# Kernel optimization log

Hardware: AMD Instinct MI355X
Metric: run time of the kernel (lower is better)

## Reference

```python
import jax, jax.numpy as jnp
import numpy as np

N = 50000      # nodes
E = 800000     # edges (before self-loops)
IN = 128       # in_channels
HID = 32       # hidden_channels per head
H = 4          # in_head
OUT = 40       # out_channels
OH = 1         # out_head
NEG = 0.2      # GATConv default negative_slope
EPS = 1e-5     # BatchNorm eps
SKIP = 0.5     # skip_coefficient


def setup_inputs() -> dict:
    key = jax.random.key(0)
    ks = jax.random.split(key, 24)
    s = 0.1
    f32 = jnp.float32
    return dict(
        x=jax.random.normal(ks[0], (N, IN), dtype=f32),
        W0=jax.random.normal(ks[1], (H * HID, IN), dtype=f32) * s,
        as0=jax.random.normal(ks[2], (H, HID), dtype=f32) * s,
        ad0=jax.random.normal(ks[3], (H, HID), dtype=f32) * s,
        b0=jnp.zeros((H * HID,), f32),
        g0=jnp.ones((H * HID,), f32),
        be0=jnp.zeros((H * HID,), f32),
        W1=jax.random.normal(ks[4], (H * HID, H * HID), dtype=f32) * s,
        as1=jax.random.normal(ks[5], (H, HID), dtype=f32) * s,
        ad1=jax.random.normal(ks[6], (H, HID), dtype=f32) * s,
        b1=jnp.zeros((H * HID,), f32),
        g1=jnp.ones((H * HID,), f32),
        be1=jnp.zeros((H * HID,), f32),
        W2=jax.random.normal(ks[7], (OH * OUT, H * HID), dtype=f32) * s,
        as2=jax.random.normal(ks[8], (OH, OUT), dtype=f32) * s,
        ad2=jax.random.normal(ks[9], (OH, OUT), dtype=f32) * s,
        b2=jnp.zeros((OH * OUT,), f32),
        edge_index=jax.random.randint(ks[10], (2, E), 0, N, dtype=jnp.int64),
    )


def gat_layer(x, src, dst, W, a_s, a_d, b, heads, ch):
    # PyG GATConv (concat=True): per-head linear, edge LeakyReLU attention,
    # softmax over incoming edges per destination node, scatter-add aggregate.
    n = x.shape[0]
    h = (x @ W.T).reshape(n, heads, ch)            # [N,H,C]
    al_s = jnp.einsum('nhc,hc->nh', h, a_s)        # [N,H]
    al_d = jnp.einsum('nhc,hc->nh', h, a_d)
    e = jax.nn.leaky_relu(al_s[src] + al_d[dst], NEG)   # [Etot,H]
    m = jax.ops.segment_max(e, dst, num_segments=n)     # per-dst max (stable softmax)
    ex = jnp.exp(e - m[dst])
    denom = jax.ops.segment_sum(ex, dst, num_segments=n)
    alpha = ex / denom[dst]                              # [Etot,H]
    out = jax.ops.segment_sum(alpha[:, :, None] * h[src], dst, num_segments=n)
    return out.reshape(n, heads * ch) + b


def batchnorm(x, g, b):
    # BatchNorm1d, batch-statistics form
    mu = x.mean(0)
    var = x.var(0)
    return (x - mu) * jax.lax.rsqrt(var + EPS) * g + b


def reference(x, W0, as0, ad0, b0, g0, be0, W1, as1, ad1, b1, g1, be1,
              W2, as2, ad2, b2, edge_index):
    loops = jnp.arange(N, dtype=edge_index.dtype)   # GATConv add_self_loops=True
    src = jnp.concatenate([edge_index[0], loops])
    dst = jnp.concatenate([edge_index[1], loops])
    h = jax.nn.relu(batchnorm(gat_layer(x, src, dst, W0, as0, ad0, b0, H, HID), g0, be0))
    skip = h
    h = gat_layer(h, src, dst, W1, as1, ad1, b1, H, HID)
    h = jax.nn.relu(batchnorm(h, g1, be1) + SKIP * skip)
    return gat_layer(h, src, dst, W2, as2, ad2, b2, OH, OUT)
```

## Files before the change

kernel.cpp:

```cpp
#include <hip/hip_runtime.h>
#include <hip/hip_bf16.h>
#include <stdint.h>

#define N_NODES 50000
#define N_EDGES 800000
#define TOT_EDGES (N_EDGES + N_NODES)
#define DIM 128
#define NEG 0.2f
#define BN_EPS 1e-5f
#define SKIPC 0.5f
#define NB 196
#define BCAP 6144
#define BINA_BLKS ((N_EDGES + 4095) / 4096)

typedef __attribute__((ext_vector_type(8))) short short8;
typedef __attribute__((ext_vector_type(4))) float f32x4;

__device__ inline float bf2f(__hip_bfloat16 v) { return __bfloat162float(v); }
__device__ inline float u16f(unsigned short u) { return __uint_as_float(((unsigned int)u) << 16); }
__device__ inline unsigned short f2bu(float f) {
    __hip_bfloat16 b = __float2bfloat16(f);
    return *(unsigned short*)&b;
}
__device__ inline void fma8(float* acc, float ex, uint4 u) {
    acc[0] += ex * u16f((unsigned short)(u.x & 0xFFFFu));
    acc[1] += ex * u16f((unsigned short)(u.x >> 16));
    acc[2] += ex * u16f((unsigned short)(u.y & 0xFFFFu));
    acc[3] += ex * u16f((unsigned short)(u.y >> 16));
    acc[4] += ex * u16f((unsigned short)(u.z & 0xFFFFu));
    acc[5] += ex * u16f((unsigned short)(u.z >> 16));
    acc[6] += ex * u16f((unsigned short)(u.w & 0xFFFFu));
    acc[7] += ex * u16f((unsigned short)(u.w >> 16));
}
__device__ inline unsigned int pk2(float a, float b) {
    return (unsigned int)f2bu(a) | ((unsigned int)f2bu(b) << 16);
}

__global__ void zero_out_k(unsigned short* out, int n) {
    int g = blockIdx.x * 256 + threadIdx.x;
    if (g < n) out[g] = 0;
}

__device__ inline void binA_body(int bid, const int* __restrict__ ei,
                                 int* __restrict__ bcnt,
                                 unsigned int* __restrict__ pairs) {
    __shared__ int cnt[NB], base[NB], cur[NB];
    __shared__ int sf;
    int t = threadIdx.x;
    if (t == 0) sf = 0;
    for (int i = t; i < NB; i += 256) cnt[i] = 0;
    __syncthreads();
    if (t < 16 && ei[2 * t + 1] != 0) atomicOr(&sf, 1);
    __syncthreads();
    int f = (sf == 0);
    int b0 = bid * 4096;
    unsigned int pk[16];
    int bk[16];
    #pragma unroll
    for (int j = 0; j < 16; ++j) {
        int g = b0 + j * 256 + t;
        bk[j] = -1;
        if (g < N_EDGES) {
            int s, d;
            if (f) { s = ei[2 * g]; d = ei[2 * (N_EDGES + g)]; }
            else   { s = ei[g];     d = ei[N_EDGES + g]; }
            if ((unsigned)d < N_NODES && (unsigned)s < N_NODES) {
                bk[j] = d >> 8;
                pk[j] = (unsigned int)s | ((unsigned int)(d & 255) << 16);
                atomicAdd(&cnt[bk[j]], 1);
            }
        }
    }
    __syncthreads();
    if (t < NB) {
        int c = cnt[t];
        base[t] = c ? atomicAdd(&bcnt[t], c) : 0;
        cur[t] = 0;
    }
    __syncthreads();
    #pragma unroll
    for (int j = 0; j < 16; ++j) {
        if (bk[j] >= 0) {
            int off = base[bk[j]] + atomicAdd(&cur[bk[j]], 1);
            if (off < BCAP) pairs[(size_t)bk[j] * BCAP + off] = pk[j];
        }
    }
}

struct PrepJobs { const void* src[13]; float* dst[13]; int n[13]; };
__device__ inline void wcvt_body(int bid,
                                 const void* __restrict__ W0,
                                 const void* __restrict__ W1,
                                 const void* __restrict__ W2,
                                 unsigned short* __restrict__ Wb0,
                                 unsigned short* __restrict__ Wb1,
                                 unsigned short* __restrict__ Wb2,
                                 const PrepJobs& jobs,
                                 int* __restrict__ fflag) {
    __shared__ int cs;
    int t = threadIdx.x;
    if (t == 0) cs = 0;
    __syncthreads();
    {
        unsigned int w = ((const unsigned int*)W0)[t];
        float v0 = u16f((unsigned short)(w & 0xFFFFu));
        float a = fabsf(v0);
        int sane = (a < 2.0f && (a > 1e-20f || v0 == 0.0f)) ? 1 : 0;
        atomicAdd(&cs, sane);
    }
    __syncthreads();
    int f = (cs >= 128) ? 1 : 0;
    if (bid == 0 && t == 0) fflag[0] = f;
    if (bid < 148) {
        int g = bid * 256 + t;
        const void* W; unsigned short* Wb; int idx;
        if (g < 16384)        { W = W0; Wb = Wb0; idx = g; }
        else if (g < 32768)   { W = W1; Wb = Wb1; idx = g - 16384; }
        else if (g < 37888)   { W = W2; Wb = Wb2; idx = g - 32768; }
        else return;
        if (f) Wb[idx] = ((const unsigned short*)W)[idx];
        else   Wb[idx] = f2bu(((const float*)W)[idx]);
    } else {
        int j = bid - 148;
        int n = jobs.n[j];
        const void* s = jobs.src[j];
        float* d = jobs.dst[j];
        for (int i = t; i < n; i += 256)
            d[i] = f ? bf2f(((const __hip_bfloat16*)s)[i]) : ((const float*)s)[i];
    }
}

__global__ __launch_bounds__(256) void fat1_k(const int* __restrict__ ei,
                                              int* __restrict__ bcnt,
                                              unsigned int* __restrict__ pairs,
                                              const void* __restrict__ W0,
                                              const void* __restrict__ W1,
                                              const void* __restrict__ W2,
                                              unsigned short* __restrict__ Wb0,
                                              unsigned short* __restrict__ Wb1,
                                              unsigned short* __restrict__ Wb2,
                                              PrepJobs jobs,
                                              int* __restrict__ fflag) {
    if (blockIdx.x < BINA_BLKS) binA_body(blockIdx.x, ei, bcnt, pairs);
    else wcvt_body(blockIdx.x - BINA_BLKS, W0, W1, W2, Wb0, Wb1, Wb2, jobs, fflag);
}

__device__ inline void binB_body(int b, const int* __restrict__ bcnt,
                                 const unsigned int* __restrict__ pairs,
                                 int* __restrict__ row_ptr,
                                 int* __restrict__ ssrc) {
    __shared__ int cntL[256], scanL[256], curL[256];
    __shared__ int sred[256];
    int t = threadIdx.x;
    int n0 = b * 256;
    int nn = min(256, N_NODES - n0);
    int cnt_b = min(bcnt[b], BCAP);
    int contrib = 0;
    if (t < b) contrib = min(bcnt[t], BCAP) + min(256, N_NODES - t * 256);
    sred[t] = contrib;
    __syncthreads();
    #pragma unroll
    for (int off = 128; off > 0; off >>= 1) {
        if (t < off) sred[t] += sred[t + off];
        __syncthreads();
    }
    int gbase = sred[0];
    if (b == NB - 1 && t == 0) row_ptr[N_NODES] = gbase + cnt_b + nn;

    const unsigned int* P = pairs + (size_t)b * BCAP;
    cntL[t] = (t < nn) ? 1 : 0;
    __syncthreads();
    for (int i = t; i < cnt_b; i += 256)
        atomicAdd(&cntL[P[i] >> 16], 1);
    __syncthreads();
    int v = cntL[t];
    scanL[t] = v;
    __syncthreads();
    for (int off = 1; off < 256; off <<= 1) {
        int x = (t >= off) ? scanL[t - off] : 0;
        __syncthreads();
        scanL[t] += x;
        __syncthreads();
    }
    int excl = scanL[t] - v;
    if (t < nn) row_ptr[n0 + t] = gbase + excl;
    curL[t] = excl;
    __syncthreads();
    if (t < nn) {
        int pos = atomicAdd(&curL[t], 1);
        ssrc[gbase + pos] = n0 + t;
    }
    for (int i = t; i < cnt_b; i += 256) {
        unsigned int p = P[i];
        int pos = atomicAdd(&curL[p >> 16], 1);
        ssrc[gbase + pos] = (int)(p & 0xFFFFu);
    }
}

__device__ inline void wext_body(int bid,
                                 unsigned short* __restrict__ Wb0,
                                 unsigned short* __restrict__ Wb1,
                                 unsigned short* __restrict__ Wb2,
                                 const float* __restrict__ pAs0, const float* __restrict__ pAd0,
                                 const float* __restrict__ pAs1, const float* __restrict__ pAd1,
                                 const float* __restrict__ pAs2, const float* __restrict__ pAd2) {
    int g = bid * 256 + threadIdx.x;
    if (g < 2048) {
        int layer = g >> 10;
        int gi = g & 1023;
        int rowq = gi >> 7;
        int k = gi & 127;
        int hh = rowq & 3, dir = rowq >> 2;
        unsigned short* Wb = layer ? Wb1 : Wb0;
        const float* p = layer ? (dir ? pAd1 : pAs1) : (dir ? pAd0 : pAs0);
        float v = 0.f;
        #pragma unroll
        for (int c = 0; c < 32; ++c)
            v += p[hh * 32 + c] * u16f(Wb[(size_t)(hh * 32 + c) * 128 + k]);
        Wb[(size_t)(128 + dir * 4 + hh) * 128 + k] = f2bu(v);
    } else if (g < 2304) {
        int gi = g - 2048;
        int dir = gi >> 7;
        int k = gi & 127;
        const float* p = dir ? pAd2 : pAs2;
        float v = 0.f;
        #pragma unroll
        for (int c = 0; c < 40; ++c)
            v += p[c] * u16f(Wb2[(size_t)c * 128 + k]);
        Wb2[(size_t)(40 + dir) * 128 + k] = f2bu(v);
    }
}

__global__ __launch_bounds__(256) void fat2_k(const int* __restrict__ bcnt,
                                              const unsigned int* __restrict__ pairs,
                                              int* __restrict__ row_ptr,
                                              int* __restrict__ ssrc,
                                              unsigned short* __restrict__ Wb0,
                                              unsigned short* __restrict__ Wb1,
                                              unsigned short* __restrict__ Wb2,
                                              const float* __restrict__ pAs0, const float* __restrict__ pAd0,
                                              const float* __restrict__ pAs1, const float* __restrict__ pAd1,
                                              const float* __restrict__ pAs2, const float* __restrict__ pAd2) {
    if (blockIdx.x < NB) binB_body(blockIdx.x, bcnt, pairs, row_ptr, ssrc);
    else wext_body(blockIdx.x - NB, Wb0, Wb1, Wb2, pAs0, pAd0, pAs1, pAd1, pAs2, pAd2);
}

template<int MT, int MV, int ALBASE, int NH, int AMODE>
__device__ inline void mfma_body(const void* __restrict__ X,
                                 const unsigned short* __restrict__ Xprev,
                                 const unsigned short* __restrict__ Wb,
                                 unsigned short* __restrict__ Y,
                                 float* __restrict__ als, float* __restrict__ ald, int n,
                                 const float* __restrict__ bnA, const float* __restrict__ gA,
                                 const float* __restrict__ beA,
                                 const float* __restrict__ bnB, const float* __restrict__ gB,
                                 const float* __restrict__ beB) {
    const int MROWS = ALBASE + 2 * NH;
    __shared__ float sAsc[128], sAsh[128], sBsc[128], sBsh[128];
    if (AMODE >= 2) {
        int t = threadIdx.x;
        const float invN = 1.f / (float)N_NODES;
        if (t < 128) {
            float mean = bnA[t] * invN;
            float var = fmaxf(bnA[128 + t] * invN - mean * mean, 0.f);
            float s = rsqrtf(var + BN_EPS) * gA[t];
            sAsc[t] = s;
            sAsh[t] = beA[t] - mean * s;
        } else if (AMODE == 3) {
            int c = t - 128;
            float mean = bnB[c] * invN;
            float var = fmaxf(bnB[128 + c] * invN - mean * mean, 0.f);
            float s = rsqrtf(var + BN_EPS) * gB[c];
            sBsc[c] = s;
            sBsh[c] = beB[c] - mean * s;
        }
        __syncthreads();
    }
    int wave = (blockIdx.x * blockDim.x + threadIdx.x) >> 6;
    int r0 = wave * 16;
    if (r0 >= n) return;
    int lane = threadIdx.x & 63;
    int m = lane & 15, quad = lane >> 4;
    f32x4 acc[MT];
    #pragma unroll
    for (int t = 0; t < MT; ++t) acc[t] = (f32x4){0.f, 0.f, 0.f, 0.f};
    int arow = min(r0 + m, n - 1);

    #pragma unroll
    for (int kc = 0; kc < 4; ++kc) {
        int k0 = kc * 32 + quad * 8;
        short8 a;
        if (AMODE == 0) {
            const float* xp = (const float*)X + (size_t)arow * 128 + k0;
            float4 x0 = *(const float4*)xp;
            float4 x1 = *(const float4*)(xp + 4);
            a[0] = (short)f2bu(x0.x); a[1] = (short)f2bu(x0.y);
            a[2] = (short)f2bu(x0.z); a[3] = (short)f2bu(x0.w);
            a[4] = (short)f2bu(x1.x); a[5] = (short)f2bu(x1.y);
            a[6] = (short)f2bu(x1.z); a[7] = (short)f2bu(x1.w);
        } else if (AMODE == 1) {
            a = *(const short8*)((const unsigned short*)X + (size_t)arow * 128 + k0);
        } else if (AMODE == 2) {
            short8 hv = *(const short8*)((const unsigned short*)X + (size_t)arow * 128 + k0);
            #pragma unroll
            for (int j = 0; j < 8; ++j) {
                float v = u16f((unsigned short)hv[j]) * sAsc[k0 + j] + sAsh[k0 + j];
                a[j] = (short)f2bu(fmaxf(v, 0.f));
            }
        } else {
            short8 hv = *(const short8*)((const unsigned short*)X + (size_t)arow * 128 + k0);
            short8 pv = *(const short8*)(Xprev + (size_t)arow * 128 + k0);
            #pragma unroll
            for (int j = 0; j < 8; ++j) {
                float v0 = fmaxf(u16f((unsigned short)pv[j]) * sBsc[k0 + j] + sBsh[k0 + j], 0.f);
                float v = u16f((unsigned short)hv[j]) * sAsc[k0 + j] + sAsh[k0 + j] + SKIPC * v0;
                a[j] = (short)f2bu(fmaxf(v, 0.f));
            }
        }
        #pragma unroll
        for (int t = 0; t < MT; ++t) {
            int col = t * 16 + m;
            short8 b;
            if (col < MROWS) b = *(const short8*)(Wb + (size_t)col * 128 + k0);
            else             b = (short8){0,0,0,0,0,0,0,0};
            acc[t] = __builtin_amdgcn_mfma_f32_16x16x32_bf16(a, b, acc[t], 0, 0, 0);
        }
    }

    #pragma unroll
    for (int t = 0; t < MT; ++t) {
        int col = t * 16 + m;
        #pragma unroll
        for (int r = 0; r < 4; ++r) {
            int row = r0 + quad * 4 + r;
            if (row >= n) continue;
            if (col < MV) {
                Y[(size_t)row * MV + col] = f2bu(acc[t][r]);
            } else if (col < ALBASE + NH) {
                als[row * NH + (col - ALBASE)] = acc[t][r];
            } else if (col < ALBASE + 2 * NH) {
                ald[row * NH + (col - ALBASE - NH)] = acc[t][r];
            }
        }
    }
}

__global__ __launch_bounds__(256) void mfma_x_k(const void* __restrict__ X,
                                                const unsigned short* __restrict__ Wb,
                                                unsigned short* __restrict__ Y,
                                                float* __restrict__ als, float* __restrict__ ald,
                                                int n, const int* __restrict__ fflag) {
    if (fflag[0]) mfma_body<9, 128, 128, 4, 1>(X, nullptr, Wb, Y, als, ald, n,
                                               nullptr, nullptr, nullptr, nullptr, nullptr, nullptr);
    else          mfma_body<9, 128, 128, 4, 0>(X, nullptr, Wb, Y, als, ald, n,
                                               nullptr, nullptr, nullptr, nullptr, nullptr, nullptr);
}

__global__ __launch_bounds__(256) void mfma_aff_k(const unsigned short* __restrict__ X,
                                                  const unsigned short* __restrict__ Wb,
                                                  unsigned short* __restrict__ Y,
                                                  float* __restrict__ als, float* __restrict__ ald,
                                                  int n,
                                                  const float* __restrict__ bn,
                                                  const float* __restrict__ g,
                                                  const float* __restrict__ be) {
    mfma_body<9, 128, 128, 4, 2>(X, nullptr, Wb, Y, als, ald, n,
                                 bn, g, be, nullptr, nullptr, nullptr);
}

__global__ __launch_bounds__(256) void mfma_affskip_k(const unsigned short* __restrict__ X,
                                                      const unsigned short* __restrict__ Xprev,
                                                      const unsigned short* __restrict__ Wb,
                                                      unsigned short* __restrict__ Y,
                                                      float* __restrict__ als, float* __restrict__ ald,
                                                      int n,
                                                      const float* __restrict__ bnA,
                                                      const float* __restrict__ gA,
                                                      const float* __restrict__ beA,
                                                      const float* __restrict__ bnB,
                                                      const float* __restrict__ gB,
                                                      const float* __restrict__ beB) {
    mfma_body<3, 40, 40, 1, 3>(X, Xprev, Wb, Y, als, ald, n,
                               bnA, gA, beA, bnB, gB, beB);
}

template<int H, int C, int LPG, int CPL, bool FINAL>
__global__ __launch_bounds__(256) void agg4_k(const unsigned short* __restrict__ hbuf,
                                              const float* __restrict__ als,
                                              const float* __restrict__ ald,
                                              const float* __restrict__ bias,
                                              const int* __restrict__ row_ptr,
                                              const int* __restrict__ ssrc,
                                              void* __restrict__ out,
                                              const int* __restrict__ fflag, int n) {
    const int HC = H * C;
    const int G = 64 / LPG;
    const int NV = CPL / 8;
    int gw = (blockIdx.x * blockDim.x + threadIdx.x) >> 6;
    if (gw >= n) return;
    int lane = threadIdx.x & 63;
    int grp = lane / LPG;
    int sl  = lane % LPG;
    int c0 = sl * CPL;
    bool act = c0 < HC;
    int hl = act ? (c0 / C) : 0;
    int d = gw;
    int beg = row_ptr[d], end = row_ptr[d + 1];
    float adh = ald[d * H + hl];

    float denom = 0.f;
    float acc[CPL];
    #pragma unroll
    for (int j = 0; j < CPL; ++j) acc[j] = 0.f;

    int i0 = beg + grp;
    bool h0 = i0 < end;
    bool h1 = (i0 + G) < end;
    bool h2 = (i0 + 2 * G) < end;
    float al0 = 0.f, al1 = 0.f, al2 = 0.f;
    uint4 u0[NV], u1[NV], u2[NV];
    if (h0) {
        int s = ssrc[i0];
        al0 = als[s * H + hl];
        if (act) {
            const uint4* hp = (const uint4*)(hbuf + (size_t)s * HC + c0);
            #pragma unroll
            for (int v = 0; v < NV; ++v) u0[v] = hp[v];
        }
    }
    if (h1) {
        int s = ssrc[i0 + G];
        al1 = als[s * H + hl];
        if (act) {
            const uint4* hp = (const uint4*)(hbuf + (size_t)s * HC + c0);
            #pragma unroll
            for (int v = 0; v < NV; ++v) u1[v] = hp[v];
        }
    }
    if (h2) {
        int s = ssrc[i0 + 2 * G];
        al2 = als[s * H + hl];
        if (act) {
            const uint4* hp = (const uint4*)(hbuf + (size_t)s * HC + c0);
            #pragma unroll
            for (int v = 0; v < NV; ++v) u2[v] = hp[v];
        }
    }
    int inext = i0 + 3 * G;

    while (h0) {
        bool h3 = inext < end;
        float al3 = 0.f;
        uint4 u3[NV];
        if (h3) {
            int s = ssrc[inext];
            al3 = als[s * H + hl];
            if (act) {
                const uint4* hp = (const uint4*)(hbuf + (size_t)s * HC + c0);
                #pragma unroll
                for (int v = 0; v < NV; ++v) u3[v] = hp[v];
            }
        }
        float t = al0 + adh;
        t = t > 0.f ? t : NEG * t;
        float ex = __expf(t);
        denom += ex;
        if (act) {
            #pragma unroll
            for (int v = 0; v < NV; ++v) fma8(acc + v * 8, ex, u0[v]);
        }
        h0 = h1; al0 = al1;
        #pragma unroll
        for (int v = 0; v < NV; ++v) u0[v] = u1[v];
        h1 = h2; al1 = al2;
        #pragma unroll
        for (int v = 0; v < NV; ++v) u1[v] = u2[v];
        h2 = h3; al2 = al3;
        #pragma unroll
        for (int v = 0; v < NV; ++v) u2[v] = u3[v];
        inext += G;
    }

    #pragma unroll
    for (int off = LPG; off < 64; off <<= 1) {
        denom += __shfl_xor(denom, off, 64);
        #pragma unroll
        for (int j = 0; j < CPL; ++j) acc[j] += __shfl_xor(acc[j], off, 64);
    }

    if (grp == 0 && act) {
        float inv = 1.f / denom;
        float vals[CPL];
        #pragma unroll
        for (int j = 0; j < CPL; ++j) vals[j] = acc[j] * inv + bias[c0 + j];
        if (FINAL && !fflag[0]) {
            float* of = (float*)out + (size_t)d * HC + c0;
            #pragma unroll
            for (int j = 0; j < CPL; ++j) of[j] = vals[j];
        } else {
            unsigned short* ob = (unsigned short*)out + (size_t)d * HC + c0;
            #pragma unroll
            for (int v = 0; v < NV; ++v) {
                uint4 pk;
                pk.x = pk2(vals[v * 8 + 0], vals[v * 8 + 1]);
                pk.y = pk2(vals[v * 8 + 2], vals[v * 8 + 3]);
                pk.z = pk2(vals[v * 8 + 4], vals[v * 8 + 5]);
                pk.w = pk2(vals[v * 8 + 6], vals[v * 8 + 7]);
                *(uint4*)(ob + v * 8) = pk;
            }
        }
    }
}

__global__ __launch_bounds__(256) void bn_stats_k(const unsigned short* __restrict__ x,
                                                  float* __restrict__ sum,
                                                  float* __restrict__ sumsq, int n) {
    __shared__ float ss[256], sq[256];
    int t = threadIdx.x;
    int c = t & 127, half = t >> 7;
    float s = 0.f, s2 = 0.f;
    for (int r = blockIdx.x * 2 + half; r < n; r += gridDim.x * 2) {
        float v = u16f(x[(size_t)r * 128 + c]);
        s += v; s2 += v * v;
    }
    ss[t] = s; sq[t] = s2;
    __syncthreads();
    if (t < 128) {
        s = ss[t] + ss[t + 128];
        s2 = sq[t] + sq[t + 128];
        atomicAdd(&sum[c], s);
        atomicAdd(&sumsq[c], s2);
    }
}

extern "C" void kernel_launch(void* const* d_in, const int* in_sizes, int n_in,
                              void* d_out, int out_size, void* d_ws, size_t ws_size,
                              hipStream_t stream) {
    const void* x   = d_in[0];
    const void* W0  = d_in[1];
    const void* as0 = d_in[2];
    const void* ad0 = d_in[3];
    const void* b0  = d_in[4];
    const void* g0  = d_in[5];
    const void* be0 = d_in[6];
    const void* W1  = d_in[7];
    const void* as1 = d_in[8];
    const void* ad1 = d_in[9];
    const void* b1  = d_in[10];
    const void* g1  = d_in[11];
    const void* be1 = d_in[12];
    const void* W2  = d_in[13];
    const void* as2 = d_in[14];
    const void* ad2 = d_in[15];
    const void* b2  = d_in[16];
    const int* ei = (const int*)d_in[17];

    char* w = (char*)d_ws;
    size_t off = 0;
    auto alloc = [&](size_t bytes) -> void* {
        void* p = w + off;
        off = (off + bytes + 255) & ~(size_t)255;
        return p;
    };
    unsigned short* hbf = (unsigned short*)alloc((size_t)N_NODES * 128 * 2);
    unsigned short* hA0 = (unsigned short*)alloc((size_t)N_NODES * 128 * 2);
    unsigned short* hA1 = (unsigned short*)alloc((size_t)N_NODES * 128 * 2);
    float* als = (float*)alloc((size_t)N_NODES * 4 * 4);
    float* ald = (float*)alloc((size_t)N_NODES * 4 * 4);
    unsigned short* Wb0 = (unsigned short*)alloc((size_t)136 * 128 * 2);
    unsigned short* Wb1 = (unsigned short*)alloc((size_t)136 * 128 * 2);
    unsigned short* Wb2 = (unsigned short*)alloc((size_t)42 * 128 * 2);
    float* prm = (float*)alloc(2048 * 4);
    int* zreg = (int*)alloc((size_t)(NB + 512) * 4);
    int* bcnt = zreg;
    float* bn0 = (float*)(zreg + NB);
    float* bn1 = bn0 + 256;
    int* row_ptr = (int*)alloc((size_t)(N_NODES + 1) * 4);
    int* ssrc    = (int*)alloc((size_t)TOT_EDGES * 4);
    unsigned int* pairs = (unsigned int*)alloc((size_t)NB * BCAP * 4);
    int* fflag   = (int*)alloc(256);

    float* pAs0 = prm + 0,   * pAd0 = prm + 128,  * pB0 = prm + 256;
    float* pG0  = prm + 384, * pBe0 = prm + 512;
    float* pAs1 = prm + 640, * pAd1 = prm + 768,  * pB1 = prm + 896;
    float* pG1  = prm + 1024,* pBe1 = prm + 1152;
    float* pAs2 = prm + 1280,* pAd2 = prm + 1320, * pB2 = prm + 1360;

    if (off > ws_size) {
        zero_out_k<<<(out_size + 255) / 256, 256, 0, stream>>>((unsigned short*)d_out, out_size);
        return;
    }

    const int MB = (((N_NODES + 15) / 16) + 3) / 4;
    const int AB = (N_NODES * 64 + 255) / 256;

    PrepJobs jobs;
    const void* srcs[13] = { as0, ad0, b0, g0, be0, as1, ad1, b1, g1, be1, as2, ad2, b2 };
    float* dsts[13] = { pAs0, pAd0, pB0, pG0, pBe0, pAs1, pAd1, pB1, pG1, pBe1, pAs2, pAd2, pB2 };
    int ns[13] = { 128,128,128,128,128, 128,128,128,128,128, 40,40,40 };
    for (int i = 0; i < 13; ++i) { jobs.src[i] = srcs[i]; jobs.dst[i] = dsts[i]; jobs.n[i] = ns[i]; }

    hipMemsetAsync(zreg, 0, (size_t)(NB + 512) * 4, stream);
    fat1_k<<<BINA_BLKS + 161, 256, 0, stream>>>(ei, bcnt, pairs, W0, W1, W2, Wb0, Wb1, Wb2, jobs, fflag);
    fat2_k<<<NB + 9, 256, 0, stream>>>(bcnt, pairs, row_ptr, ssrc, Wb0, Wb1, Wb2,
                                       pAs0, pAd0, pAs1, pAd1, pAs2, pAd2);
    mfma_x_k<<<MB, 256, 0, stream>>>(x, Wb0, hbf, als, ald, N_NODES, fflag);
    agg4_k<4, 32, 8, 16, false><<<AB, 256, 0, stream>>>(hbf, als, ald, pB0, row_ptr, ssrc, hA0, fflag, N_NODES);
    bn_stats_k<<<256, 256, 0, stream>>>(hA0, bn0, bn0 + 128, N_NODES);
    mfma_aff_k<<<MB, 256, 0, stream>>>(hA0, Wb1, hbf, als, ald, N_NODES, bn0, pG0, pBe0);
    agg4_k<4, 32, 8, 16, false><<<AB, 256, 0, stream>>>(hbf, als, ald, pB1, row_ptr, ssrc, hA1, fflag, N_NODES);
    bn_stats_k<<<256, 256, 0, stream>>>(hA1, bn1, bn1 + 128, N_NODES);
    mfma_affskip_k<<<MB, 256, 0, stream>>>(hA1, hA0, Wb2, hbf, als, ald, N_NODES,
                                           bn1, pG1, pBe1, bn0, pG0, pBe0);
    agg4_k<1, 40, 8, 8, true><<<AB, 256, 0, stream>>>(hbf, als, ald, pB2, row_ptr, ssrc, d_out, fflag, N_NODES);
}
```

Before: 348.3 us.

## Split node features into two 64-column slabs and aggregate each slab per XCD

```diff
diff --git a/kernel.cpp b/kernel.cpp
--- a/kernel.cpp
+++ b/kernel.cpp
@@ -12,6 +12,7 @@
 #define NB 196
 #define BCAP 6144
 #define BINA_BLKS ((N_EDGES + 4095) / 4096)
+#define AGGS_BLKS (((N_NODES + 3) / 4) * 2)
 
 typedef __attribute__((ext_vector_type(8))) short short8;
 typedef __attribute__((ext_vector_type(4))) float f32x4;
@@ -301,15 +302,21 @@
         } else if (AMODE == 1) {
             a = *(const short8*)((const unsigned short*)X + (size_t)arow * 128 + k0);
         } else if (AMODE == 2) {
-            short8 hv = *(const short8*)((const unsigned short*)X + (size_t)arow * 128 + k0);
+            const unsigned short* xs = (const unsigned short*)X +
+                ((size_t)(k0 >> 6) * n + arow) * 64 + (k0 & 63);
+            short8 hv = *(const short8*)xs;
             #pragma unroll
             for (int j = 0; j < 8; ++j) {
                 float v = u16f((unsigned short)hv[j]) * sAsc[k0 + j] + sAsh[k0 + j];
                 a[j] = (short)f2bu(fmaxf(v, 0.f));
             }
         } else {
-            short8 hv = *(const short8*)((const unsigned short*)X + (size_t)arow * 128 + k0);
-            short8 pv = *(const short8*)(Xprev + (size_t)arow * 128 + k0);
+            const unsigned short* xs = (const unsigned short*)X +
+                ((size_t)(k0 >> 6) * n + arow) * 64 + (k0 & 63);
+            const unsigned short* xps = Xprev +
+                ((size_t)(k0 >> 6) * n + arow) * 64 + (k0 & 63);
+            short8 hv = *(const short8*)xs;
+            short8 pv = *(const short8*)xps;
             #pragma unroll
             for (int j = 0; j < 8; ++j) {
                 float v0 = fmaxf(u16f((unsigned short)pv[j]) * sBsc[k0 + j] + sBsh[k0 + j], 0.f);
@@ -335,7 +342,10 @@
             int row = r0 + quad * 4 + r;
             if (row >= n) continue;
             if (col < MV) {
-                Y[(size_t)row * MV + col] = f2bu(acc[t][r]);
+                if (MV == 128)
+                    Y[((size_t)(col >> 6) * n + row) * 64 + (col & 63)] = f2bu(acc[t][r]);
+                else
+                    Y[(size_t)row * MV + col] = f2bu(acc[t][r]);
             } else if (col < ALBASE + NH) {
                 als[row * NH + (col - ALBASE)] = acc[t][r];
             } else if (col < ALBASE + 2 * NH) {
@@ -382,6 +392,85 @@
                                                       const float* __restrict__ beB) {
     mfma_body<3, 40, 40, 1, 3>(X, Xprev, Wb, Y, als, ald, n,
                                bnA, gA, beA, bnB, gB, beB);
+}
+
+__global__ __launch_bounds__(256) void aggsplit_k(const unsigned short* __restrict__ hbuf,
+                                                  const float* __restrict__ als,
+                                                  const float* __restrict__ ald,
+                                                  const float* __restrict__ bias,
+                                                  const int* __restrict__ row_ptr,
+                                                  const int* __restrict__ ssrc,
+                                                  unsigned short* __restrict__ out,
+                                                  int n) {
+    const int G = 8;
+    int b = blockIdx.x;
+    int xcd = b & 7;
+    int hp = xcd >> 2;
+    int jb = (b >> 3) * 4 + (xcd & 3);
+    int w = threadIdx.x >> 6;
+    int d = jb * 4 + w;
+    if (d >= n) return;
+    int lane = threadIdx.x & 63;
+    int grp = lane >> 3;
+    int sl = lane & 7;
+    int c0 = sl * 8;
+    int hl = hp * 2 + (sl >> 2);
+    const unsigned short* hb = hbuf + (size_t)hp * n * 64;
+    int beg = row_ptr[d], end = row_ptr[d + 1];
+    float adh = ald[d * 4 + hl];
+
+    float denom = 0.f;
+    float acc[8];
+    #pragma unroll
+    for (int j = 0; j < 8; ++j) acc[j] = 0.f;
+
+    int i0 = beg + grp;
+    bool h0 = i0 < end;
+    bool h1 = (i0 + G) < end;
+    bool h2 = (i0 + 2 * G) < end;
+    float al0 = 0.f, al1 = 0.f, al2 = 0.f;
+    uint4 u0, u1, u2;
+    if (h0) { int s = ssrc[i0];         al0 = als[s * 4 + hl]; u0 = *(const uint4*)(hb + (size_t)s * 64 + c0); }
+    if (h1) { int s = ssrc[i0 + G];     al1 = als[s * 4 + hl]; u1 = *(const uint4*)(hb + (size_t)s * 64 + c0); }
+    if (h2) { int s = ssrc[i0 + 2 * G]; al2 = als[s * 4 + hl]; u2 = *(const uint4*)(hb + (size_t)s * 64 + c0); }
+    int inext = i0 + 3 * G;
+
+    while (h0) {
+        bool h3 = inext < end;
+        float al3 = 0.f;
+        uint4 u3;
+        if (h3) { int s = ssrc[inext]; al3 = als[s * 4 + hl]; u3 = *(const uint4*)(hb + (size_t)s * 64 + c0); }
+        float t = al0 + adh;
+        t = t > 0.f ? t : NEG * t;
+        float ex = __expf(t);
+        denom += ex;
+        fma8(acc, ex, u0);
+        h0 = h1; al0 = al1; u0 = u1;
+        h1 = h2; al1 = al2; u1 = u2;
+        h2 = h3; al2 = al3; u2 = u3;
+        inext += G;
+    }
+
+    #pragma unroll
+    for (int off = 8; off < 64; off <<= 1) {
+        denom += __shfl_xor(denom, off, 64);
+        #pragma unroll
+        for (int j = 0; j < 8; ++j) acc[j] += __shfl_xor(acc[j], off, 64);
+    }
+
+    if (grp == 0) {
+        float inv = 1.f / denom;
+        float vals[8];
+        #pragma unroll
+        for (int j = 0; j < 8; ++j) vals[j] = acc[j] * inv + bias[hp * 64 + c0 + j];
+        unsigned short* ob = out + ((size_t)hp * n + d) * 64 + c0;
+        uint4 pk;
+        pk.x = pk2(vals[0], vals[1]);
+        pk.y = pk2(vals[2], vals[3]);
+        pk.z = pk2(vals[4], vals[5]);
+        pk.w = pk2(vals[6], vals[7]);
+        *(uint4*)ob = pk;
+    }
 }
 
 template<int H, int C, int LPG, int CPL, bool FINAL>
@@ -518,9 +607,11 @@
     __shared__ float ss[256], sq[256];
     int t = threadIdx.x;
     int c = t & 127, half = t >> 7;
+    int slab = c >> 6, col = c & 63;
+    const unsigned short* xs = x + (size_t)slab * n * 64 + col;
     float s = 0.f, s2 = 0.f;
     for (int r = blockIdx.x * 2 + half; r < n; r += gridDim.x * 2) {
-        float v = u16f(x[(size_t)r * 128 + c]);
+        float v = u16f(xs[(size_t)r * 64]);
         s += v; s2 += v * v;
     }
     ss[t] = s; sq[t] = s2;
@@ -605,10 +696,10 @@
     fat2_k<<<NB + 9, 256, 0, stream>>>(bcnt, pairs, row_ptr, ssrc, Wb0, Wb1, Wb2,
                                        pAs0, pAd0, pAs1, pAd1, pAs2, pAd2);
     mfma_x_k<<<MB, 256, 0, stream>>>(x, Wb0, hbf, als, ald, N_NODES, fflag);
-    agg4_k<4, 32, 8, 16, false><<<AB, 256, 0, stream>>>(hbf, als, ald, pB0, row_ptr, ssrc, hA0, fflag, N_NODES);
+    aggsplit_k<<<AGGS_BLKS, 256, 0, stream>>>(hbf, als, ald, pB0, row_ptr, ssrc, hA0, N_NODES);
     bn_stats_k<<<256, 256, 0, stream>>>(hA0, bn0, bn0 + 128, N_NODES);
     mfma_aff_k<<<MB, 256, 0, stream>>>(hA0, Wb1, hbf, als, ald, N_NODES, bn0, pG0, pBe0);
-    agg4_k<4, 32, 8, 16, false><<<AB, 256, 0, stream>>>(hbf, als, ald, pB1, row_ptr, ssrc, hA1, fflag, N_NODES);
+    aggsplit_k<<<AGGS_BLKS, 256, 0, stream>>>(hbf, als, ald, pB1, row_ptr, ssrc, hA1, N_NODES);
     bn_stats_k<<<256, 256, 0, stream>>>(hA1, bn1, bn1 + 128, N_NODES);
     mfma_affskip_k<<<MB, 256, 0, stream>>>(hA1, hA0, Wb2, hbf, als, ald, N_NODES,
                                            bn1, pG1, pBe1, bn0, pG0, pBe0);
```

Measured after the change: 363.7 us. 1.04x slower.
